# Kernel tuning notes

Measured on AMD Instinct MI355X. Metric: run time of the kernel, lower is better.

## Reference

```python
import jax, jax.numpy as jnp
import numpy as np

EPS = 1e-5

def _layernorm(x, w, b):
    mu = jnp.mean(x, axis=-1, keepdims=True)
    var = jnp.mean(jnp.square(x - mu), axis=-1, keepdims=True)
    return (x - mu) * jax.lax.rsqrt(var + EPS) * w + b

def setup_inputs() -> dict:
    key = jax.random.key(0)
    ks = jax.random.split(key, 8)
    B, N, C, D = 32, 1024, 4096, 64
    x = jax.random.normal(ks[0], (B, N, C), dtype=jnp.float32)
    gumbel = jax.random.gumbel(ks[1], (B, N, 2), dtype=jnp.float32)
    ln_w = jnp.ones((C,), jnp.float32)
    ln_b = jnp.zeros((C,), jnp.float32)
    w1 = jax.random.normal(ks[2], (C, D), dtype=jnp.float32) * 0.02
    b1 = jnp.zeros((D,), jnp.float32)
    w2 = jax.random.normal(ks[3], (D, 2), dtype=jnp.float32) * 0.02
    b2 = jnp.zeros((2,), jnp.float32)
    return {"x": x, "gumbel": gumbel, "ln_w": ln_w, "ln_b": ln_b,
            "w1": w1, "b1": b1, "w2": w2, "b2": b2}

def reference(x, gumbel, ln_w, ln_b, w1, b1, w2, b2):
    B, N, C = x.shape
    xn = _layernorm(x, ln_w, ln_b)
    local_x = xn[:, :, : C // 2]                      # [B, N, C/2]
    # policy is all-ones -> weighted mean over tokens
    global_x = jnp.mean(xn[:, :, C // 2:], axis=1, keepdims=True)  # [B, 1, C/2]
    feat = jnp.concatenate(
        [local_x, jnp.broadcast_to(global_x, local_x.shape)], axis=-1)  # [B, N, C]
    h = jax.nn.gelu(feat @ w1 + b1, approximate=False)  # [B, N, 64]
    logits = h @ w2 + b2                                # [B, N, 2]
    pred_score = jax.nn.log_softmax(logits, axis=-1)
    # gumbel-softmax (tau=1, hard=True) with straight-through estimator
    y_soft = jax.nn.softmax(pred_score + gumbel, axis=-1)
    hard = jax.nn.one_hot(jnp.argmax(y_soft, axis=-1), 2, dtype=y_soft.dtype)
    y = hard - jax.lax.stop_gradient(y_soft) + y_soft
    keep = y[:, :, 0]                                   # [B, N]
    # dense equivalent of masked_select/split: zero out dropped tokens
    return x * keep[:, :, None]
```

## Files before the change

kernel.cpp:

```cpp
#include <hip/hip_runtime.h>
#include <math.h>

#define B_   32
#define N_   1024
#define C_   4096
#define HC_  2048
#define D_   64
#define NT_  32768
#define KS_  4
#define KC_  (HC_ / KS_)
#define BKC_ 32

__device__ __forceinline__ float4 ld4(const float* p) {
    return *reinterpret_cast<const float4*>(p);
}

__global__ __launch_bounds__(256) void k3_fused(
        const float* __restrict__ x, const float* __restrict__ lnw,
        const float* __restrict__ w1, float* __restrict__ Pp,
        float* __restrict__ spq) {
    __shared__ float As[BKC_ * 256];
    __shared__ float Bsm[BKC_ * D_];

    const int t = threadIdx.x;
    const int mt = blockIdx.x & 127;
    const int ks = blockIdx.x >> 7;
    const int T0 = mt * 256;
    const int kbase = ks * KC_;
    const int rt = t & 63;
    const int dt = t >> 6;
    const int lrow = t >> 3;
    const int lq = t & 7;

    float acc[64];
#pragma unroll
    for (int i = 0; i < 64; ++i) acc[i] = 0.f;
    float sRow[8], qRow[8];
#pragma unroll
    for (int p = 0; p < 8; ++p) { sRow[p] = 0.f; qRow[p] = 0.f; }

    float4 xv[8];
    float4 wv1, wv2;
    float lw1, lw2;
    {
        const int k0 = kbase;
#pragma unroll
        for (int p = 0; p < 8; ++p)
            xv[p] = ld4(x + (size_t)(T0 + lrow + 32 * p) * C_ + k0 + lq * 4);
        const float4* s4 = reinterpret_cast<const float4*>(
            w1 + (size_t)k0 * D_);
        wv1 = s4[t]; wv2 = s4[256 + t];
        lw1 = lnw[k0 + (t >> 4)];
        lw2 = lnw[k0 + 16 + (t >> 4)];
    }

#pragma unroll 1
    for (int kc = 0; kc < KC_ / BKC_; ++kc) {
#pragma unroll
        for (int p = 0; p < 8; ++p) {
            const float4 v = xv[p];
            const int r = lrow + 32 * p;
            const int g = r >> 2, rm = r & 3;
            const int kb = 4 * lq;
            As[(kb + 0) * 256 + (((g ^ ((kb + 0) & 7)) << 2) + rm)] = v.x;
            As[(kb + 1) * 256 + (((g ^ ((kb + 1) & 7)) << 2) + rm)] = v.y;
            As[(kb + 2) * 256 + (((g ^ ((kb + 2) & 7)) << 2) + rm)] = v.z;
            As[(kb + 3) * 256 + (((g ^ ((kb + 3) & 7)) << 2) + rm)] = v.w;
            sRow[p] += (v.x + v.y) + (v.z + v.w);
            qRow[p] = fmaf(v.x, v.x, fmaf(v.y, v.y,
                      fmaf(v.z, v.z, fmaf(v.w, v.w, qRow[p]))));
        }
        {
            float4 v1 = wv1, v2 = wv2;
            v1.x *= lw1; v1.y *= lw1; v1.z *= lw1; v1.w *= lw1;
            v2.x *= lw2; v2.y *= lw2; v2.z *= lw2; v2.w *= lw2;
            float4* b4 = reinterpret_cast<float4*>(Bsm);
            b4[t] = v1;
            b4[256 + t] = v2;
        }
        __syncthreads();
        if (kc + 1 < KC_ / BKC_) {
            const int k1 = kbase + (kc + 1) * BKC_;
#pragma unroll
            for (int p = 0; p < 8; ++p)
                xv[p] = ld4(x + (size_t)(T0 + lrow + 32 * p) * C_
                            + k1 + lq * 4);
            const float4* s4 = reinterpret_cast<const float4*>(
                w1 + (size_t)k1 * D_);
            wv1 = s4[t]; wv2 = s4[256 + t];
            lw1 = lnw[k1 + (t >> 4)];
            lw2 = lnw[k1 + 16 + (t >> 4)];
        }
#pragma unroll 4
        for (int k = 0; k < BKC_; ++k) {
            const float4 a4 = *reinterpret_cast<const float4*>(
                As + k * 256 + ((rt ^ (k & 7)) << 2));
            const float* br = Bsm + k * D_ + dt * 16;
            const float4 b0 = ld4(br), b1 = ld4(br + 4),
                         b2 = ld4(br + 8), b3 = ld4(br + 12);
            const float av[4] = {a4.x, a4.y, a4.z, a4.w};
            const float bv[16] = {b0.x, b0.y, b0.z, b0.w,
                                  b1.x, b1.y, b1.z, b1.w,
                                  b2.x, b2.y, b2.z, b2.w,
                                  b3.x, b3.y, b3.z, b3.w};
#pragma unroll
            for (int ri = 0; ri < 4; ++ri)
#pragma unroll
                for (int cj = 0; cj < 16; ++cj)
                    acc[ri * 16 + cj] =
                        fmaf(av[ri], bv[cj], acc[ri * 16 + cj]);
        }
        __syncthreads();
    }
#pragma unroll
    for (int ri = 0; ri < 4; ++ri) {
        float* dst = Pp + ((size_t)ks * NT_ + T0 + rt * 4 + ri) * D_ + dt * 16;
#pragma unroll
        for (int c = 0; c < 4; ++c)
            *reinterpret_cast<float4*>(dst + c * 4) = make_float4(
                acc[ri * 16 + c * 4], acc[ri * 16 + c * 4 + 1],
                acc[ri * 16 + c * 4 + 2], acc[ri * 16 + c * 4 + 3]);
    }
#pragma unroll
    for (int p = 0; p < 8; ++p) {
        float s = sRow[p], q = qRow[p];
        s += __shfl_xor(s, 1); q += __shfl_xor(q, 1);
        s += __shfl_xor(s, 2); q += __shfl_xor(q, 2);
        s += __shfl_xor(s, 4); q += __shfl_xor(q, 4);
        if (lq == 0) {
            const size_t r = (size_t)(T0 + lrow + 32 * p) * 8;
            spq[r + ks] = s;
            spq[r + 4 + ks] = q;
        }
    }
}

__global__ __launch_bounds__(256) void k1_upper(
        const float* __restrict__ x, const float* __restrict__ lnw,
        const float* __restrict__ lnb, const float* __restrict__ spq,
        float* __restrict__ muv, float* __restrict__ rsv,
        float* __restrict__ part) {
    __shared__ float sh[4][HC_];
    const int t = threadIdx.x;
    const int lane = t & 63, w = t >> 6;
    const int bid = blockIdx.x;
    const int b = bid >> 5;
    const int g = bid & 31;

    float4 wv[8], bv[8], gacc[8];
#pragma unroll
    for (int m = 0; m < 8; ++m) {
        wv[m] = ld4(lnw + HC_ + (m * 64 + lane) * 4);
        bv[m] = ld4(lnb + HC_ + (m * 64 + lane) * 4);
        gacc[m] = make_float4(0.f, 0.f, 0.f, 0.f);
    }

    for (int i = 0; i < 8; ++i) {
        const int tok = b * N_ + g * 32 + w * 8 + i;
        const float* row = x + (size_t)tok * C_ + HC_;
        float4 v[8];
        float s = 0.f, q = 0.f;
#pragma unroll
        for (int m = 0; m < 8; ++m) {
            v[m] = ld4(row + (m * 64 + lane) * 4);
            s += (v[m].x + v[m].y) + (v[m].z + v[m].w);
            q = fmaf(v[m].x, v[m].x, fmaf(v[m].y, v[m].y,
                fmaf(v[m].z, v[m].z, fmaf(v[m].w, v[m].w, q))));
        }
#pragma unroll
        for (int o = 1; o < 64; o <<= 1) {
            s += __shfl_xor(s, o);
            q += __shfl_xor(q, o);
        }
        const float4 s0 = ld4(spq + (size_t)tok * 8);
        const float4 q0 = ld4(spq + (size_t)tok * 8 + 4);
        const float S = s + (s0.x + s0.y) + (s0.z + s0.w);
        const float Q = q + (q0.x + q0.y) + (q0.z + q0.w);
        const float mu = S * (1.f / C_);
        const float rs = rsqrtf(Q * (1.f / C_) - mu * mu + 1e-5f);
        if (lane == 0) {
            muv[tok] = mu;
            rsv[tok] = rs;
        }
#pragma unroll
        for (int m = 0; m < 8; ++m) {
            gacc[m].x += (v[m].x - mu) * rs * wv[m].x + bv[m].x;
            gacc[m].y += (v[m].y - mu) * rs * wv[m].y + bv[m].y;
            gacc[m].z += (v[m].z - mu) * rs * wv[m].z + bv[m].z;
            gacc[m].w += (v[m].w - mu) * rs * wv[m].w + bv[m].w;
        }
    }
#pragma unroll
    for (int m = 0; m < 8; ++m)
        *reinterpret_cast<float4*>(&sh[w][(m * 64 + lane) * 4]) = gacc[m];
    __syncthreads();
    float* pp = part + (size_t)bid * HC_;
#pragma unroll
    for (int m = 0; m < 8; ++m) {
        const int j = (m * 64 + lane) * 4;
        const float4 a0 = ld4(&sh[0][j]);
        const float4 a1 = ld4(&sh[1][j]);
        const float4 a2 = ld4(&sh[2][j]);
        const float4 a3 = ld4(&sh[3][j]);
        float4 r;
        r.x = (a0.x + a1.x) + (a2.x + a3.x);
        r.y = (a0.y + a1.y) + (a2.y + a3.y);
        r.z = (a0.z + a1.z) + (a2.z + a3.z);
        r.w = (a0.w + a1.w) + (a2.w + a3.w);
        if (w == (m & 3))
            *reinterpret_cast<float4*>(pp + j) = r;
    }
}

__global__ __launch_bounds__(256) void k2a_part(
        const float* __restrict__ part, const float* __restrict__ w1,
        const float* __restrict__ lnw, const float* __restrict__ lnb,
        float* __restrict__ gpart, float* __restrict__ Wpart,
        float* __restrict__ Bpart) {
    __shared__ float Gs[256];
    __shared__ float red[2][4][64];
    const int t = threadIdx.x;
    const int d = t & 63, s = t >> 6;
    const int blk = blockIdx.x;
    if (blk < 256) {
        const int b = blk >> 3, jq = blk & 7;
        const int j = jq * 256 + t;
        float a = 0.f;
        for (int k = 0; k < 32; ++k)
            a += part[(size_t)(b * 32 + k) * HC_ + j];
        Gs[t] = a;
        __syncthreads();
        float acc = 0.f;
        const int j0 = jq * 256 + s * 64;
        for (int jj = 0; jj < 64; ++jj)
            acc = fmaf(Gs[s * 64 + jj],
                       w1[(size_t)(HC_ + j0 + jj) * D_ + d], acc);
        red[0][s][d] = acc;
        __syncthreads();
        if (s == 0)
            gpart[(size_t)blk * 64 + d] =
                red[0][0][d] + red[0][1][d] + red[0][2][d] + red[0][3][d];
    } else {
        const int wq = blk - 256;
        const int c0 = wq * 256 + s * 64;
        float a = 0.f, c2 = 0.f;
        for (int c = c0; c < c0 + 64; ++c) {
            const float wvv = w1[(size_t)c * D_ + d];
            a = fmaf(lnw[c], wvv, a);
            c2 = fmaf(lnb[c], wvv, c2);
        }
        red[0][s][d] = a;
        red[1][s][d] = c2;
        __syncthreads();
        if (s == 0) {
            Wpart[wq * 64 + d] =
                red[0][0][d] + red[0][1][d] + red[0][2][d] + red[0][3][d];
            Bpart[wq * 64 + d] =
                red[1][0][d] + red[1][1][d] + red[1][2][d] + red[1][3][d];
        }
    }
}

__global__ __launch_bounds__(64) void k2b_final(
        const float* __restrict__ gpart, const float* __restrict__ Wpart,
        const float* __restrict__ Bpart, float* __restrict__ gterm,
        float* __restrict__ W1s, float* __restrict__ Bs) {
    const int d = threadIdx.x;
    const int b = blockIdx.x;
    if (b < B_) {
        float a = 0.f;
#pragma unroll
        for (int q = 0; q < 8; ++q)
            a += gpart[(size_t)(b * 8 + q) * 64 + d];
        gterm[b * D_ + d] = a * (1.f / N_);
    } else {
        float a = 0.f, c2 = 0.f;
#pragma unroll
        for (int q = 0; q < 8; ++q) {
            a += Wpart[q * 64 + d];
            c2 += Bpart[q * 64 + d];
        }
        W1s[d] = a;
        Bs[d] = c2;
    }
}

__global__ __launch_bounds__(256) void k45_decide_mask(
        const float* __restrict__ Pp, const float* __restrict__ muv,
        const float* __restrict__ rsv, const float* __restrict__ gterm,
        const float* __restrict__ W1s, const float* __restrict__ Bs,
        const float* __restrict__ b1, const float* __restrict__ w2,
        const float* __restrict__ b2, const float* __restrict__ gum,
        const float* __restrict__ x, float* __restrict__ out) {
    const int t = threadIdx.x;
    const int lane = t & 63, w = t >> 6;
    const int token = blockIdx.x * 4 + w;
    const int b = token >> 10;

    const float2 gv = *reinterpret_cast<const float2*>(gum + token * 2);
    float p = 0.f;
#pragma unroll
    for (int s = 0; s < KS_; ++s)
        p += Pp[((size_t)s * NT_ + token) * D_ + lane];

    const float mu = muv[token], rs = rsv[token];
    float h = rs * (p - mu * W1s[lane]) + Bs[lane] + gterm[b * D_ + lane]
              + b1[lane];
    h = 0.5f * h * (1.f + erff(h * 0.70710678118654752f));
    const float2 w2v = *reinterpret_cast<const float2*>(w2 + lane * 2);
    float l0 = h * w2v.x;
    float l1 = h * w2v.y;
#pragma unroll
    for (int o = 1; o < 64; o <<= 1) {
        l0 += __shfl_xor(l0, o);
        l1 += __shfl_xor(l1, o);
    }
    const float z0 = l0 + b2[0] + gv.x;
    const float z1 = l1 + b2[1] + gv.y;

    float4* dst = reinterpret_cast<float4*>(out + (size_t)token * C_);
    if (z0 >= z1) {
        const float4* src =
            reinterpret_cast<const float4*>(x + (size_t)token * C_);
#pragma unroll
        for (int c = 0; c < 16; ++c)
            dst[c * 64 + lane] = src[c * 64 + lane];
    } else {
        const float4 z = make_float4(0.f, 0.f, 0.f, 0.f);
#pragma unroll
        for (int c = 0; c < 16; ++c)
            dst[c * 64 + lane] = z;
    }
}

extern "C" void kernel_launch(void* const* d_in, const int* in_sizes, int n_in,
                              void* d_out, int out_size, void* d_ws,
                              size_t ws_size, hipStream_t stream) {
    const float* x   = (const float*)d_in[0];
    const float* gum = (const float*)d_in[1];
    const float* lnw = (const float*)d_in[2];
    const float* lnb = (const float*)d_in[3];
    const float* w1  = (const float*)d_in[4];
    const float* b1  = (const float*)d_in[5];
    const float* w2  = (const float*)d_in[6];
    const float* b2  = (const float*)d_in[7];
    float* out = (float*)d_out;

    float* wsf   = (float*)d_ws;
    float* Pp    = wsf;
    float* muv   = Pp + (size_t)KS_ * NT_ * D_;
    float* rsv   = muv + NT_;
    float* part  = rsv + NT_;
    float* gterm = part + (size_t)1024 * HC_;
    float* W1s   = gterm + B_ * D_;
    float* Bs    = W1s + D_;
    float* spq   = Bs + D_;
    float* gpart = spq + (size_t)NT_ * 8;
    float* Wpart = gpart + 256 * 64;
    float* Bpart = Wpart + 8 * 64;

    k3_fused<<<KS_ * 128, 256, 0, stream>>>(x, lnw, w1, Pp, spq);
    k1_upper<<<1024, 256, 0, stream>>>(x, lnw, lnb, spq, muv, rsv, part);
    k2a_part<<<264, 256, 0, stream>>>(part, w1, lnw, lnb,
                                      gpart, Wpart, Bpart);
    k2b_final<<<33, 64, 0, stream>>>(gpart, Wpart, Bpart, gterm, W1s, Bs);
    k45_decide_mask<<<NT_ / 4, 256, 0, stream>>>(Pp, muv, rsv, gterm, W1s,
                                                 Bs, b1, w2, b2, gum, x, out);
}
```

Before: 407.7 us.

## Fuse all stages into one cooperative persistent kernel with grid syncs

Merges the five separate kernels into a single cooperative kernel that loops over tiles per phase and uses grid-wide syncs between phases, with a fallback to the old multi-kernel path. It also halves the number of upper-half partial groups (64 tokens per group instead of 32), which shrinks the partial buffer and the reduction work. The aim is to remove kernel launch gaps and tail effects between stages. In exchange, the grid is capped by occupancy and the phases are serialized by grid barriers, so any phase with fewer jobs than blocks leaves blocks idle.

```diff
diff --git a/kernel.cpp b/kernel.cpp
--- a/kernel.cpp
+++ b/kernel.cpp
@@ -1,5 +1,8 @@
 #include <hip/hip_runtime.h>
+#include <hip/hip_cooperative_groups.h>
 #include <math.h>
+
+namespace cg = cooperative_groups;
 
 #define B_   32
 #define N_   1024
@@ -15,16 +18,14 @@
     return *reinterpret_cast<const float4*>(p);
 }
 
-__global__ __launch_bounds__(256) void k3_fused(
+
+__device__ __forceinline__ void p0_gemm_tile(
+        int tileId, int t, float* As, float* Bsm,
         const float* __restrict__ x, const float* __restrict__ lnw,
         const float* __restrict__ w1, float* __restrict__ Pp,
         float* __restrict__ spq) {
-    __shared__ float As[BKC_ * 256];
-    __shared__ float Bsm[BKC_ * D_];
-
-    const int t = threadIdx.x;
-    const int mt = blockIdx.x & 127;
-    const int ks = blockIdx.x >> 7;
+    const int mt = tileId & 127;
+    const int ks = tileId >> 7;
     const int T0 = mt * 256;
     const int kbase = ks * KC_;
     const int rt = t & 63;
@@ -96,13 +97,13 @@
             const float4 a4 = *reinterpret_cast<const float4*>(
                 As + k * 256 + ((rt ^ (k & 7)) << 2));
             const float* br = Bsm + k * D_ + dt * 16;
-            const float4 b0 = ld4(br), b1 = ld4(br + 4),
-                         b2 = ld4(br + 8), b3 = ld4(br + 12);
+            const float4 b0 = ld4(br), b1v = ld4(br + 4),
+                         b2v = ld4(br + 8), b3v = ld4(br + 12);
             const float av[4] = {a4.x, a4.y, a4.z, a4.w};
             const float bv[16] = {b0.x, b0.y, b0.z, b0.w,
-                                  b1.x, b1.y, b1.z, b1.w,
-                                  b2.x, b2.y, b2.z, b2.w,
-                                  b3.x, b3.y, b3.z, b3.w};
+                                  b1v.x, b1v.y, b1v.z, b1v.w,
+                                  b2v.x, b2v.y, b2v.z, b2v.w,
+                                  b3v.x, b3v.y, b3v.z, b3v.w};
 #pragma unroll
             for (int ri = 0; ri < 4; ++ri)
 #pragma unroll
@@ -135,18 +136,15 @@
     }
 }
 
-__global__ __launch_bounds__(256) void k1_upper(
+__device__ __forceinline__ void p1_upper_group(
+        int u, int t, float* As ,
         const float* __restrict__ x, const float* __restrict__ lnw,
         const float* __restrict__ lnb, const float* __restrict__ spq,
         float* __restrict__ muv, float* __restrict__ rsv,
         float* __restrict__ part) {
-    __shared__ float sh[4][HC_];
-    const int t = threadIdx.x;
     const int lane = t & 63, w = t >> 6;
-    const int bid = blockIdx.x;
-    const int b = bid >> 5;
-    const int g = bid & 31;
-
+    const int b = u >> 4;
+    const int g = u & 15;
     float4 wv[8], bv[8], gacc[8];
 #pragma unroll
     for (int m = 0; m < 8; ++m) {
@@ -154,9 +152,8 @@
         bv[m] = ld4(lnb + HC_ + (m * 64 + lane) * 4);
         gacc[m] = make_float4(0.f, 0.f, 0.f, 0.f);
     }
-
-    for (int i = 0; i < 8; ++i) {
-        const int tok = b * N_ + g * 32 + w * 8 + i;
+    for (int i = 0; i < 16; ++i) {
+        const int tok = b * N_ + g * 64 + w * 16 + i;
         const float* row = x + (size_t)tok * C_ + HC_;
         float4 v[8];
         float s = 0.f, q = 0.f;
@@ -190,11 +187,13 @@
             gacc[m].w += (v[m].w - mu) * rs * wv[m].w + bv[m].w;
         }
     }
+    float (*sh)[HC_] = reinterpret_cast<float(*)[HC_]>(As);
+    __syncthreads();
 #pragma unroll
     for (int m = 0; m < 8; ++m)
         *reinterpret_cast<float4*>(&sh[w][(m * 64 + lane) * 4]) = gacc[m];
     __syncthreads();
-    float* pp = part + (size_t)bid * HC_;
+    float* pp = part + (size_t)u * HC_;
 #pragma unroll
     for (int m = 0; m < 8; ++m) {
         const int j = (m * 64 + lane) * 4;
@@ -212,53 +211,186 @@
     }
 }
 
+__device__ __forceinline__ void p2_job(
+        int job, int t, float* Gs, float* red, int nPartPerBatch,
+        const float* __restrict__ part, const float* __restrict__ w1,
+        const float* __restrict__ lnw, const float* __restrict__ lnb,
+        float* __restrict__ gpart, float* __restrict__ Wpart,
+        float* __restrict__ Bpart) {
+    const int d = t & 63, s = t >> 6;
+    if (job < 256) {
+        const int b = job >> 3, jq = job & 7;
+        const int j = jq * 256 + t;
+        float a = 0.f;
+        for (int k = 0; k < nPartPerBatch; ++k)
+            a += part[(size_t)(b * nPartPerBatch + k) * HC_ + j];
+        Gs[t] = a;
+        __syncthreads();
+        float acc = 0.f;
+        const int j0 = jq * 256 + s * 64;
+        for (int jj = 0; jj < 64; ++jj)
+            acc = fmaf(Gs[s * 64 + jj],
+                       w1[(size_t)(HC_ + j0 + jj) * D_ + d], acc);
+        red[s * 64 + d] = acc;
+        __syncthreads();
+        if (s == 0)
+            gpart[(size_t)job * 64 + d] =
+                red[d] + red[64 + d] + red[128 + d] + red[192 + d];
+        __syncthreads();
+    } else {
+        const int wq = job - 256;
+        const int c0 = wq * 256 + s * 64;
+        float a = 0.f, c2 = 0.f;
+        for (int c = c0; c < c0 + 64; ++c) {
+            const float wvv = w1[(size_t)c * D_ + d];
+            a = fmaf(lnw[c], wvv, a);
+            c2 = fmaf(lnb[c], wvv, c2);
+        }
+        red[s * 64 + d] = a;
+        red[256 + s * 64 + d] = c2;
+        __syncthreads();
+        if (s == 0) {
+            Wpart[wq * 64 + d] =
+                red[d] + red[64 + d] + red[128 + d] + red[192 + d];
+            Bpart[wq * 64 + d] = red[256 + d] + red[320 + d]
+                               + red[384 + d] + red[448 + d];
+        }
+        __syncthreads();
+    }
+}
+
+__device__ __forceinline__ void p4_token(
+        int token, int lane,
+        const float* __restrict__ Pp, const float* __restrict__ muv,
+        const float* __restrict__ rsv, const float* __restrict__ gterm,
+        const float* __restrict__ W1s, const float* __restrict__ Bs,
+        const float* __restrict__ b1, const float* __restrict__ w2,
+        const float* __restrict__ b2, const float* __restrict__ gum,
+        const float* __restrict__ x, float* __restrict__ out) {
+    const int b = token >> 10;
+    const float2 gv = *reinterpret_cast<const float2*>(gum + token * 2);
+    float p = 0.f;
+#pragma unroll
+    for (int s = 0; s < KS_; ++s)
+        p += Pp[((size_t)s * NT_ + token) * D_ + lane];
+
+    const float mu = muv[token], rs = rsv[token];
+    float h = rs * (p - mu * W1s[lane]) + Bs[lane] + gterm[b * D_ + lane]
+              + b1[lane];
+    h = 0.5f * h * (1.f + erff(h * 0.70710678118654752f));
+    const float2 w2v = *reinterpret_cast<const float2*>(w2 + lane * 2);
+    float l0 = h * w2v.x;
+    float l1 = h * w2v.y;
+#pragma unroll
+    for (int o = 1; o < 64; o <<= 1) {
+        l0 += __shfl_xor(l0, o);
+        l1 += __shfl_xor(l1, o);
+    }
+    const float z0 = l0 + b2[0] + gv.x;
+    const float z1 = l1 + b2[1] + gv.y;
+
+    float4* dst = reinterpret_cast<float4*>(out + (size_t)token * C_);
+    if (z0 >= z1) {
+        const float4* src =
+            reinterpret_cast<const float4*>(x + (size_t)token * C_);
+#pragma unroll
+        for (int c = 0; c < 16; ++c)
+            dst[c * 64 + lane] = src[c * 64 + lane];
+    } else {
+        const float4 z = make_float4(0.f, 0.f, 0.f, 0.f);
+#pragma unroll
+        for (int c = 0; c < 16; ++c)
+            dst[c * 64 + lane] = z;
+    }
+}
+
+__global__ __launch_bounds__(256) void mega(
+        const float* __restrict__ x, const float* __restrict__ gum,
+        const float* __restrict__ lnw, const float* __restrict__ lnb,
+        const float* __restrict__ w1, const float* __restrict__ b1,
+        const float* __restrict__ w2, const float* __restrict__ b2,
+        float* __restrict__ out, float* __restrict__ Pp,
+        float* __restrict__ muv, float* __restrict__ rsv,
+        float* __restrict__ part, float* __restrict__ gterm,
+        float* __restrict__ W1s, float* __restrict__ Bs,
+        float* __restrict__ spq, float* __restrict__ gpart,
+        float* __restrict__ Wpart, float* __restrict__ Bpart) {
+    __shared__ float As[BKC_ * 256];
+    __shared__ float Bsm[BKC_ * D_];
+
+    cg::grid_group grid = cg::this_grid();
+    const int t = threadIdx.x;
+    const int bid = blockIdx.x;
+    const int NB = gridDim.x;
+    const int lane = t & 63, w = t >> 6;
+
+    for (int tile = bid; tile < 512; tile += NB)
+        p0_gemm_tile(tile, t, As, Bsm, x, lnw, w1, Pp, spq);
+    grid.sync();
+
+    for (int u = bid; u < 512; u += NB)
+        p1_upper_group(u, t, As, x, lnw, lnb, spq, muv, rsv, part);
+    grid.sync();
+
+    for (int job = bid; job < 264; job += NB)
+        p2_job(job, t, Bsm, Bsm + 256, 16, part, w1, lnw, lnb,
+               gpart, Wpart, Bpart);
+    grid.sync();
+
+    for (int j = bid; j < 33; j += NB) {
+        if (j < B_ && t < 64) {
+            float a = 0.f;
+#pragma unroll
+            for (int q = 0; q < 8; ++q)
+                a += gpart[(size_t)(j * 8 + q) * 64 + t];
+            gterm[j * D_ + t] = a * (1.f / N_);
+        } else if (j == B_ && t < 64) {
+            float a = 0.f, c2 = 0.f;
+#pragma unroll
+            for (int q = 0; q < 8; ++q) {
+                a += Wpart[q * 64 + t];
+                c2 += Bpart[q * 64 + t];
+            }
+            W1s[t] = a;
+            Bs[t] = c2;
+        }
+    }
+    grid.sync();
+
+    for (int u = bid; u < 512; u += NB)
+        for (int i = 0; i < 16; ++i)
+            p4_token(u * 64 + w * 16 + i, lane, Pp, muv, rsv, gterm,
+                     W1s, Bs, b1, w2, b2, gum, x, out);
+}
+
+__global__ __launch_bounds__(256) void k3_fused(
+        const float* __restrict__ x, const float* __restrict__ lnw,
+        const float* __restrict__ w1, float* __restrict__ Pp,
+        float* __restrict__ spq) {
+    __shared__ float As[BKC_ * 256];
+    __shared__ float Bsm[BKC_ * D_];
+    p0_gemm_tile(blockIdx.x, threadIdx.x, As, Bsm, x, lnw, w1, Pp, spq);
+}
+
+__global__ __launch_bounds__(256) void k1_upper(
+        const float* __restrict__ x, const float* __restrict__ lnw,
+        const float* __restrict__ lnb, const float* __restrict__ spq,
+        float* __restrict__ muv, float* __restrict__ rsv,
+        float* __restrict__ part) {
+    __shared__ float As[BKC_ * 256];
+    p1_upper_group(blockIdx.x, threadIdx.x, As, x, lnw, lnb, spq,
+                   muv, rsv, part);
+}
+
 __global__ __launch_bounds__(256) void k2a_part(
         const float* __restrict__ part, const float* __restrict__ w1,
         const float* __restrict__ lnw, const float* __restrict__ lnb,
         float* __restrict__ gpart, float* __restrict__ Wpart,
         float* __restrict__ Bpart) {
     __shared__ float Gs[256];
-    __shared__ float red[2][4][64];
-    const int t = threadIdx.x;
-    const int d = t & 63, s = t >> 6;
-    const int blk = blockIdx.x;
-    if (blk < 256) {
-        const int b = blk >> 3, jq = blk & 7;
-        const int j = jq * 256 + t;
-        float a = 0.f;
-        for (int k = 0; k < 32; ++k)
-            a += part[(size_t)(b * 32 + k) * HC_ + j];
-        Gs[t] = a;
-        __syncthreads();
-        float acc = 0.f;
-        const int j0 = jq * 256 + s * 64;
-        for (int jj = 0; jj < 64; ++jj)
-            acc = fmaf(Gs[s * 64 + jj],
-                       w1[(size_t)(HC_ + j0 + jj) * D_ + d], acc);
-        red[0][s][d] = acc;
-        __syncthreads();
-        if (s == 0)
-            gpart[(size_t)blk * 64 + d] =
-                red[0][0][d] + red[0][1][d] + red[0][2][d] + red[0][3][d];
-    } else {
-        const int wq = blk - 256;
-        const int c0 = wq * 256 + s * 64;
-        float a = 0.f, c2 = 0.f;
-        for (int c = c0; c < c0 + 64; ++c) {
-            const float wvv = w1[(size_t)c * D_ + d];
-            a = fmaf(lnw[c], wvv, a);
-            c2 = fmaf(lnb[c], wvv, c2);
-        }
-        red[0][s][d] = a;
-        red[1][s][d] = c2;
-        __syncthreads();
-        if (s == 0) {
-            Wpart[wq * 64 + d] =
-                red[0][0][d] + red[0][1][d] + red[0][2][d] + red[0][3][d];
-            Bpart[wq * 64 + d] =
-                red[1][0][d] + red[1][1][d] + red[1][2][d] + red[1][3][d];
-        }
-    }
+    __shared__ float red[512];
+    p2_job(blockIdx.x, threadIdx.x, Gs, red, 16, part, w1, lnw, lnb,
+           gpart, Wpart, Bpart);
 }
 
 __global__ __launch_bounds__(64) void k2b_final(
@@ -292,45 +424,9 @@
         const float* __restrict__ b1, const float* __restrict__ w2,
         const float* __restrict__ b2, const float* __restrict__ gum,
         const float* __restrict__ x, float* __restrict__ out) {
-    const int t = threadIdx.x;
-    const int lane = t & 63, w = t >> 6;
-    const int token = blockIdx.x * 4 + w;
-    const int b = token >> 10;
-
-    const float2 gv = *reinterpret_cast<const float2*>(gum + token * 2);
-    float p = 0.f;
-#pragma unroll
-    for (int s = 0; s < KS_; ++s)
-        p += Pp[((size_t)s * NT_ + token) * D_ + lane];
-
-    const float mu = muv[token], rs = rsv[token];
-    float h = rs * (p - mu * W1s[lane]) + Bs[lane] + gterm[b * D_ + lane]
-              + b1[lane];
-    h = 0.5f * h * (1.f + erff(h * 0.70710678118654752f));
-    const float2 w2v = *reinterpret_cast<const float2*>(w2 + lane * 2);
-    float l0 = h * w2v.x;
-    float l1 = h * w2v.y;
-#pragma unroll
-    for (int o = 1; o < 64; o <<= 1) {
-        l0 += __shfl_xor(l0, o);
-        l1 += __shfl_xor(l1, o);
-    }
-    const float z0 = l0 + b2[0] + gv.x;
-    const float z1 = l1 + b2[1] + gv.y;
-
-    float4* dst = reinterpret_cast<float4*>(out + (size_t)token * C_);
-    if (z0 >= z1) {
-        const float4* src =
-            reinterpret_cast<const float4*>(x + (size_t)token * C_);
-#pragma unroll
-        for (int c = 0; c < 16; ++c)
-            dst[c * 64 + lane] = src[c * 64 + lane];
-    } else {
-        const float4 z = make_float4(0.f, 0.f, 0.f, 0.f);
-#pragma unroll
-        for (int c = 0; c < 16; ++c)
-            dst[c * 64 + lane] = z;
-    }
+    const int lane = threadIdx.x & 63, w = threadIdx.x >> 6;
+    p4_token(blockIdx.x * 4 + w, lane, Pp, muv, rsv, gterm, W1s, Bs,
+             b1, w2, b2, gum, x, out);
 }
 
 extern "C" void kernel_launch(void* const* d_in, const int* in_sizes, int n_in,
@@ -351,7 +447,7 @@
     float* muv   = Pp + (size_t)KS_ * NT_ * D_;
     float* rsv   = muv + NT_;
     float* part  = rsv + NT_;
-    float* gterm = part + (size_t)1024 * HC_;
+    float* gterm = part + (size_t)512 * HC_;
     float* W1s   = gterm + B_ * D_;
     float* Bs    = W1s + D_;
     float* spq   = Bs + D_;
@@ -359,8 +455,37 @@
     float* Wpart = gpart + 256 * 64;
     float* Bpart = Wpart + 8 * 64;
 
+    int dev = 0;
+    (void)hipGetDevice(&dev);
+    int coop = 0, numCU = 0;
+    (void)hipDeviceGetAttribute(&coop, hipDeviceAttributeCooperativeLaunch,
+                                dev);
+    (void)hipDeviceGetAttribute(&numCU,
+                                hipDeviceAttributeMultiprocessorCount, dev);
+    if (coop && numCU > 0) {
+        int maxBlk = 0;
+        hipError_t oe = hipOccupancyMaxActiveBlocksPerMultiprocessor(
+            &maxBlk, (const void*)mega, 256, 0);
+        if (oe == hipSuccess && maxBlk >= 1) {
+            int gridSz = maxBlk * numCU;
+            if (gridSz > 512) gridSz = 512;
+            void* args[] = {
+                (void*)&x, (void*)&gum, (void*)&lnw, (void*)&lnb,
+                (void*)&w1, (void*)&b1, (void*)&w2, (void*)&b2,
+                (void*)&out, (void*)&Pp, (void*)&muv, (void*)&rsv,
+                (void*)&part, (void*)&gterm, (void*)&W1s, (void*)&Bs,
+                (void*)&spq, (void*)&gpart, (void*)&Wpart, (void*)&Bpart};
+            hipError_t le = hipLaunchCooperativeKernel(
+                (void*)mega, dim3(gridSz), dim3(256), args, 0, stream);
+            if (le == hipSuccess) return;
+            (void)hipGetLastError();
+        } else {
+            (void)hipGetLastError();
+        }
+    }
+
     k3_fused<<<KS_ * 128, 256, 0, stream>>>(x, lnw, w1, Pp, spq);
-    k1_upper<<<1024, 256, 0, stream>>>(x, lnw, lnb, spq, muv, rsv, part);
+    k1_upper<<<512, 256, 0, stream>>>(x, lnw, lnb, spq, muv, rsv, part);
     k2a_part<<<264, 256, 0, stream>>>(part, w1, lnw, lnb,
                                       gpart, Wpart, Bpart);
     k2b_final<<<33, 64, 0, stream>>>(gpart, Wpart, Bpart, gterm, W1s, Bs);
```

New measurement: 539.0 us. 1.32x slower.

## Halve k3 row tile to 128 tokens and double grid with new LDS swizzle

Applied to the files above, without the earlier changes.

The fused LN-stats plus GEMM kernel now handles 128 tokens per block instead of 256. Each thread keeps 32 accumulators instead of 64, and the grid grows from 512 to 1024 blocks. This is meant to lower register pressure, raise occupancy and fill the GPU's compute units better. The A-tile LDS swizzle is redone to stay conflict-free for the narrower layout, at the cost of more w1 tile reloads per token. k2a's reduction array is flattened, which does not change its work.

```diff
diff --git a/kernel.cpp b/kernel.cpp
--- a/kernel.cpp
+++ b/kernel.cpp
@@ -19,33 +19,33 @@
         const float* __restrict__ x, const float* __restrict__ lnw,
         const float* __restrict__ w1, float* __restrict__ Pp,
         float* __restrict__ spq) {
-    __shared__ float As[BKC_ * 256];
+    __shared__ float As[BKC_ * 128];
     __shared__ float Bsm[BKC_ * D_];
 
     const int t = threadIdx.x;
-    const int mt = blockIdx.x & 127;
-    const int ks = blockIdx.x >> 7;
-    const int T0 = mt * 256;
+    const int mt = blockIdx.x & 255;
+    const int ks = blockIdx.x >> 8;
+    const int T0 = mt * 128;
     const int kbase = ks * KC_;
-    const int rt = t & 63;
-    const int dt = t >> 6;
+    const int rt = t & 31;
+    const int dt = t >> 5;
     const int lrow = t >> 3;
     const int lq = t & 7;
 
-    float acc[64];
-#pragma unroll
-    for (int i = 0; i < 64; ++i) acc[i] = 0.f;
-    float sRow[8], qRow[8];
-#pragma unroll
-    for (int p = 0; p < 8; ++p) { sRow[p] = 0.f; qRow[p] = 0.f; }
-
-    float4 xv[8];
+    float acc[32];
+#pragma unroll
+    for (int i = 0; i < 32; ++i) acc[i] = 0.f;
+    float sRow[4], qRow[4];
+#pragma unroll
+    for (int p = 0; p < 4; ++p) { sRow[p] = 0.f; qRow[p] = 0.f; }
+
+    float4 xv[4];
     float4 wv1, wv2;
     float lw1, lw2;
     {
         const int k0 = kbase;
 #pragma unroll
-        for (int p = 0; p < 8; ++p)
+        for (int p = 0; p < 4; ++p)
             xv[p] = ld4(x + (size_t)(T0 + lrow + 32 * p) * C_ + k0 + lq * 4);
         const float4* s4 = reinterpret_cast<const float4*>(
             w1 + (size_t)k0 * D_);
@@ -57,15 +57,18 @@
 #pragma unroll 1
     for (int kc = 0; kc < KC_ / BKC_; ++kc) {
 #pragma unroll
-        for (int p = 0; p < 8; ++p) {
+        for (int p = 0; p < 4; ++p) {
             const float4 v = xv[p];
             const int r = lrow + 32 * p;
-            const int g = r >> 2, rm = r & 3;
+            const int gq = r >> 2, rm = r & 3;
             const int kb = 4 * lq;
-            As[(kb + 0) * 256 + (((g ^ ((kb + 0) & 7)) << 2) + rm)] = v.x;
-            As[(kb + 1) * 256 + (((g ^ ((kb + 1) & 7)) << 2) + rm)] = v.y;
-            As[(kb + 2) * 256 + (((g ^ ((kb + 2) & 7)) << 2) + rm)] = v.z;
-            As[(kb + 3) * 256 + (((g ^ ((kb + 3) & 7)) << 2) + rm)] = v.w;
+#pragma unroll
+            for (int j = 0; j < 4; ++j) {
+                const float c = (j == 0) ? v.x : (j == 1) ? v.y
+                              : (j == 2) ? v.z : v.w;
+                const int p5 = (5 * lq + j) & 31;
+                As[(kb + j) * 128 + (((gq ^ p5) << 2) + rm)] = c;
+            }
             sRow[p] += (v.x + v.y) + (v.z + v.w);
             qRow[p] = fmaf(v.x, v.x, fmaf(v.y, v.y,
                       fmaf(v.z, v.z, fmaf(v.w, v.w, qRow[p]))));
@@ -82,7 +85,7 @@
         if (kc + 1 < KC_ / BKC_) {
             const int k1 = kbase + (kc + 1) * BKC_;
 #pragma unroll
-            for (int p = 0; p < 8; ++p)
+            for (int p = 0; p < 4; ++p)
                 xv[p] = ld4(x + (size_t)(T0 + lrow + 32 * p) * C_
                             + k1 + lq * 4);
             const float4* s4 = reinterpret_cast<const float4*>(
@@ -91,38 +94,37 @@
             lw1 = lnw[k1 + (t >> 4)];
             lw2 = lnw[k1 + 16 + (t >> 4)];
         }
-#pragma unroll 4
+#pragma unroll 8
         for (int k = 0; k < BKC_; ++k) {
+            const int p5 = (5 * (k >> 2) + (k & 3)) & 31;
             const float4 a4 = *reinterpret_cast<const float4*>(
-                As + k * 256 + ((rt ^ (k & 7)) << 2));
-            const float* br = Bsm + k * D_ + dt * 16;
-            const float4 b0 = ld4(br), b1 = ld4(br + 4),
-                         b2 = ld4(br + 8), b3 = ld4(br + 12);
+                As + k * 128 + ((rt ^ p5) << 2));
+            const float* br = Bsm + k * D_ + dt * 8;
+            const float4 b0 = ld4(br), b1v = ld4(br + 4);
             const float av[4] = {a4.x, a4.y, a4.z, a4.w};
-            const float bv[16] = {b0.x, b0.y, b0.z, b0.w,
-                                  b1.x, b1.y, b1.z, b1.w,
-                                  b2.x, b2.y, b2.z, b2.w,
-                                  b3.x, b3.y, b3.z, b3.w};
+            const float bv[8] = {b0.x, b0.y, b0.z, b0.w,
+                                 b1v.x, b1v.y, b1v.z, b1v.w};
 #pragma unroll
             for (int ri = 0; ri < 4; ++ri)
 #pragma unroll
-                for (int cj = 0; cj < 16; ++cj)
-                    acc[ri * 16 + cj] =
-                        fmaf(av[ri], bv[cj], acc[ri * 16 + cj]);
+                for (int cj = 0; cj < 8; ++cj)
+                    acc[ri * 8 + cj] =
+                        fmaf(av[ri], bv[cj], acc[ri * 8 + cj]);
         }
         __syncthreads();
     }
 #pragma unroll
     for (int ri = 0; ri < 4; ++ri) {
-        float* dst = Pp + ((size_t)ks * NT_ + T0 + rt * 4 + ri) * D_ + dt * 16;
-#pragma unroll
-        for (int c = 0; c < 4; ++c)
-            *reinterpret_cast<float4*>(dst + c * 4) = make_float4(
-                acc[ri * 16 + c * 4], acc[ri * 16 + c * 4 + 1],
-                acc[ri * 16 + c * 4 + 2], acc[ri * 16 + c * 4 + 3]);
-    }
-#pragma unroll
-    for (int p = 0; p < 8; ++p) {
+        float* dst = Pp + ((size_t)ks * NT_ + T0 + rt * 4 + ri) * D_ + dt * 8;
+        *reinterpret_cast<float4*>(dst) = make_float4(
+            acc[ri * 8 + 0], acc[ri * 8 + 1], acc[ri * 8 + 2],
+            acc[ri * 8 + 3]);
+        *reinterpret_cast<float4*>(dst + 4) = make_float4(
+            acc[ri * 8 + 4], acc[ri * 8 + 5], acc[ri * 8 + 6],
+            acc[ri * 8 + 7]);
+    }
+#pragma unroll
+    for (int p = 0; p < 4; ++p) {
         float s = sRow[p], q = qRow[p];
         s += __shfl_xor(s, 1); q += __shfl_xor(q, 1);
         s += __shfl_xor(s, 2); q += __shfl_xor(q, 2);
@@ -218,7 +220,7 @@
         float* __restrict__ gpart, float* __restrict__ Wpart,
         float* __restrict__ Bpart) {
     __shared__ float Gs[256];
-    __shared__ float red[2][4][64];
+    __shared__ float red[512];
     const int t = threadIdx.x;
     const int d = t & 63, s = t >> 6;
     const int blk = blockIdx.x;
@@ -235,11 +237,11 @@
         for (int jj = 0; jj < 64; ++jj)
             acc = fmaf(Gs[s * 64 + jj],
                        w1[(size_t)(HC_ + j0 + jj) * D_ + d], acc);
-        red[0][s][d] = acc;
+        red[s * 64 + d] = acc;
         __syncthreads();
         if (s == 0)
             gpart[(size_t)blk * 64 + d] =
-                red[0][0][d] + red[0][1][d] + red[0][2][d] + red[0][3][d];
+                red[d] + red[64 + d] + red[128 + d] + red[192 + d];
     } else {
         const int wq = blk - 256;
         const int c0 = wq * 256 + s * 64;
@@ -249,14 +251,14 @@
             a = fmaf(lnw[c], wvv, a);
             c2 = fmaf(lnb[c], wvv, c2);
         }
-        red[0][s][d] = a;
-        red[1][s][d] = c2;
+        red[s * 64 + d] = a;
+        red[256 + s * 64 + d] = c2;
         __syncthreads();
         if (s == 0) {
             Wpart[wq * 64 + d] =
-                red[0][0][d] + red[0][1][d] + red[0][2][d] + red[0][3][d];
-            Bpart[wq * 64 + d] =
-                red[1][0][d] + red[1][1][d] + red[1][2][d] + red[1][3][d];
+                red[d] + red[64 + d] + red[128 + d] + red[192 + d];
+            Bpart[wq * 64 + d] = red[256 + d] + red[320 + d]
+                               + red[384 + d] + red[448 + d];
         }
     }
 }
@@ -359,7 +361,7 @@
     float* Wpart = gpart + 256 * 64;
     float* Bpart = Wpart + 8 * 64;
 
-    k3_fused<<<KS_ * 128, 256, 0, stream>>>(x, lnw, w1, Pp, spq);
+    k3_fused<<<KS_ * 256, 256, 0, stream>>>(x, lnw, w1, Pp, spq);
     k1_upper<<<1024, 256, 0, stream>>>(x, lnw, lnb, spq, muv, rsv, part);
     k2a_part<<<264, 256, 0, stream>>>(part, w1, lnw, lnb,
                                       gpart, Wpart, Bpart);
```

Measured after the change: 398.1 us. 1.02x faster.
